# Kernel tuning notes

Hardware: AMD Instinct MI355X
Metric: run time of the kernel (lower is better)

## Reference

```python
import jax, jax.numpy as jnp
import numpy as np
from math import sqrt

B, IN_F, OUT_F = 32, 1024, 4096
DROPOUT_RATE = 0.1


def setup_inputs() -> dict:
    key = jax.random.key(0)
    kx, kw, kb, kmw, kmb = jax.random.split(key, 5)
    k = sqrt(1.0 / IN_F)  # He-style init std from source
    x = jax.random.normal(kx, (B, IN_F), dtype=jnp.float32)
    weight = k * jax.random.normal(kw, (IN_F, OUT_F), dtype=jnp.float32)
    bias = k * jax.random.normal(kb, (OUT_F,), dtype=jnp.float32)
    # per-sample Bernoulli keep masks: rand > dropout_rate (no 1/(1-p) rescale in source)
    w_mask = jax.random.uniform(kmw, (B, IN_F, OUT_F)) > DROPOUT_RATE
    b_mask = jax.random.uniform(kmb, (B, OUT_F)) > DROPOUT_RATE
    return {"x": x, "weight": weight, "bias": bias, "w_mask": w_mask, "b_mask": b_mask}


def reference(x, weight, bias, w_mask, b_mask):
    # 'w' dropout mode: per-sample masked weight matmul, vectorized over batch
    # (replaces the original Python loop of B GEMVs with one batched contraction).
    mw = w_mask.astype(x.dtype)
    y = jnp.einsum("bi,io,bio->bo", x, weight, mw)  # [B, OUT_F]
    return y + bias[None, :] * b_mask.astype(x.dtype)
```

## Files before the change

### kernel.cpp

```cpp
#include <hip/hip_runtime.h>


#define B_DIM 32
#define IN_F 1024
#define OUT_F 4096
#define N_CHUNK 4
#define I_CHUNK (IN_F / N_CHUNK)
#define BO (B_DIM * OUT_F)

typedef int   v4i __attribute__((ext_vector_type(4)));
typedef float v4f __attribute__((ext_vector_type(4)));

__global__ __launch_bounds__(256, 2) void masked_gemv_partial(
    const float* __restrict__ x,
    const float* __restrict__ weight,
    const int* __restrict__ w_mask,
    float* __restrict__ partial)
{
    const int bid   = blockIdx.x;
    const int b     = bid >> 4;
    const int s     = bid & 15;
    const int o_blk = s >> 2;
    const int chunk = s & 3;
    const int i0    = chunk * I_CHUNK;
    const int o     = o_blk * 1024 + (threadIdx.x << 2);

    __shared__ float xs[I_CHUNK];
    xs[threadIdx.x] = x[b * IN_F + i0 + threadIdx.x];
    __syncthreads();

    const int*   mptr = w_mask + (size_t)b * IN_F * OUT_F + (size_t)i0 * OUT_F + o;
    const float* wptr = weight + (size_t)i0 * OUT_F + o;

    v4f acc = {0.f, 0.f, 0.f, 0.f};
#pragma unroll 8
    for (int i = 0; i < I_CHUNK; ++i) {
        const float xi = xs[i];
        const v4i m = __builtin_nontemporal_load((const v4i*)(mptr + (size_t)i * OUT_F));
        const v4f w = *(const v4f*)(wptr + (size_t)i * OUT_F);
        acc.x = fmaf(xi * (float)m.x, w.x, acc.x);
        acc.y = fmaf(xi * (float)m.y, w.y, acc.y);
        acc.z = fmaf(xi * (float)m.z, w.z, acc.z);
        acc.w = fmaf(xi * (float)m.w, w.w, acc.w);
    }

    __builtin_nontemporal_store(acc,
        (v4f*)(partial + (size_t)chunk * BO + b * OUT_F + o));
}

__global__ __launch_bounds__(256) void reduce_bias_kernel(
    const float* __restrict__ partial,
    const float* __restrict__ bias,
    const int* __restrict__ b_mask,
    float* __restrict__ out)
{
    const int tid = blockIdx.x * 256 + threadIdx.x;
    float s0 = partial[tid]               + partial[(size_t)1 * BO + tid];
    float s1 = partial[(size_t)2 * BO + tid] + partial[(size_t)3 * BO + tid];
    const int o = tid & (OUT_F - 1);
    out[tid] = fmaf(bias[o], (float)b_mask[tid], s0 + s1);
}

extern "C" void kernel_launch(void* const* d_in, const int* in_sizes, int n_in,
                              void* d_out, int out_size, void* d_ws, size_t ws_size,
                              hipStream_t stream) {
    const float* x      = (const float*)d_in[0];
    const float* weight = (const float*)d_in[1];
    const float* bias   = (const float*)d_in[2];
    const int*   w_mask = (const int*)d_in[3];
    const int*   b_mask = (const int*)d_in[4];
    float* out     = (float*)d_out;
    float* partial = (float*)d_ws;

    masked_gemv_partial<<<B_DIM * 16, 256, 0, stream>>>(x, weight, w_mask, partial);
    reduce_bias_kernel<<<BO / 256, 256, 0, stream>>>(partial, bias, b_mask, out);
}
```

Baseline: 679.0 us.

## Share weight loads across batch groups and split input dimension into more chunks

Each block now covers 8 batch samples instead of one, so every weight row segment it loads is reused for 8 masked accumulations rather than being read separately per sample. The input dimension is split into 32 chunks instead of 4, giving 512 blocks of short loops. The reduce kernel is vectorized to sum 32 partials with float4 loads. The workload is dominated by the 512MB mask stream, so weight reuse saves little bandwidth, while the partial buffer grows eightfold and each thread now holds 32 accumulator registers.

```diff
diff --git a/kernel.cpp b/kernel.cpp
--- a/kernel.cpp
+++ b/kernel.cpp
@@ -4,7 +4,9 @@
 #define B_DIM 32
 #define IN_F 1024
 #define OUT_F 4096
-#define N_CHUNK 4
+#define BGRP 8
+#define NBG (B_DIM / BGRP)
+#define N_CHUNK 32
 #define I_CHUNK (IN_F / N_CHUNK)
 #define BO (B_DIM * OUT_F)
 
@@ -18,34 +20,48 @@
     float* __restrict__ partial)
 {
     const int bid   = blockIdx.x;
-    const int b     = bid >> 4;
-    const int s     = bid & 15;
-    const int o_blk = s >> 2;
-    const int chunk = s & 3;
+    const int bgrp  = bid >> 7;
+    const int o_blk = (bid >> 5) & 3;
+    const int chunk = bid & 31;
+    const int b0    = bgrp * BGRP;
     const int i0    = chunk * I_CHUNK;
     const int o     = o_blk * 1024 + (threadIdx.x << 2);
 
-    __shared__ float xs[I_CHUNK];
-    xs[threadIdx.x] = x[b * IN_F + i0 + threadIdx.x];
+    __shared__ float xs[BGRP][I_CHUNK];
+    {
+        const int bb = threadIdx.x >> 5;
+        const int ii = threadIdx.x & 31;
+        xs[bb][ii] = x[(b0 + bb) * IN_F + i0 + ii];
+    }
     __syncthreads();
 
-    const int*   mptr = w_mask + (size_t)b * IN_F * OUT_F + (size_t)i0 * OUT_F + o;
     const float* wptr = weight + (size_t)i0 * OUT_F + o;
+    const int*   mbase = w_mask + ((size_t)b0 * IN_F + i0) * OUT_F + o;
 
-    v4f acc = {0.f, 0.f, 0.f, 0.f};
-#pragma unroll 8
+    v4f acc[BGRP];
+#pragma unroll
+    for (int bb = 0; bb < BGRP; ++bb) acc[bb] = (v4f){0.f, 0.f, 0.f, 0.f};
+
+#pragma unroll 2
     for (int i = 0; i < I_CHUNK; ++i) {
-        const float xi = xs[i];
-        const v4i m = __builtin_nontemporal_load((const v4i*)(mptr + (size_t)i * OUT_F));
         const v4f w = *(const v4f*)(wptr + (size_t)i * OUT_F);
-        acc.x = fmaf(xi * (float)m.x, w.x, acc.x);
-        acc.y = fmaf(xi * (float)m.y, w.y, acc.y);
-        acc.z = fmaf(xi * (float)m.z, w.z, acc.z);
-        acc.w = fmaf(xi * (float)m.w, w.w, acc.w);
+#pragma unroll
+        for (int bb = 0; bb < BGRP; ++bb) {
+            const v4i m = __builtin_nontemporal_load(
+                (const v4i*)(mbase + ((size_t)bb * IN_F + i) * OUT_F));
+            const float xi = xs[bb][i];
+            acc[bb].x = fmaf(xi * (float)m.x, w.x, acc[bb].x);
+            acc[bb].y = fmaf(xi * (float)m.y, w.y, acc[bb].y);
+            acc[bb].z = fmaf(xi * (float)m.z, w.z, acc[bb].z);
+            acc[bb].w = fmaf(xi * (float)m.w, w.w, acc[bb].w);
+        }
     }
 
-    __builtin_nontemporal_store(acc,
-        (v4f*)(partial + (size_t)chunk * BO + b * OUT_F + o));
+#pragma unroll
+    for (int bb = 0; bb < BGRP; ++bb) {
+        __builtin_nontemporal_store(acc[bb],
+            (v4f*)(partial + (size_t)chunk * BO + (b0 + bb) * OUT_F + o));
+    }
 }
 
 __global__ __launch_bounds__(256) void reduce_bias_kernel(
@@ -55,10 +71,21 @@
     float* __restrict__ out)
 {
     const int tid = blockIdx.x * 256 + threadIdx.x;
-    float s0 = partial[tid]               + partial[(size_t)1 * BO + tid];
-    float s1 = partial[(size_t)2 * BO + tid] + partial[(size_t)3 * BO + tid];
-    const int o = tid & (OUT_F - 1);
-    out[tid] = fmaf(bias[o], (float)b_mask[tid], s0 + s1);
+    const v4f* p4 = (const v4f*)partial;
+    v4f s = {0.f, 0.f, 0.f, 0.f};
+#pragma unroll
+    for (int c = 0; c < N_CHUNK; ++c) {
+        const v4f v = p4[(size_t)c * (BO / 4) + tid];
+        s.x += v.x; s.y += v.y; s.z += v.z; s.w += v.w;
+    }
+    const v4i bm = ((const v4i*)b_mask)[tid];
+    const v4f bi = ((const v4f*)bias)[tid & (OUT_F / 4 - 1)];
+    v4f r;
+    r.x = fmaf(bi.x, (float)bm.x, s.x);
+    r.y = fmaf(bi.y, (float)bm.y, s.y);
+    r.z = fmaf(bi.z, (float)bm.z, s.z);
+    r.w = fmaf(bi.w, (float)bm.w, s.w);
+    ((v4f*)out)[tid] = r;
 }
 
 extern "C" void kernel_launch(void* const* d_in, const int* in_sizes, int n_in,
@@ -72,6 +99,6 @@
     float* out     = (float*)d_out;
     float* partial = (float*)d_ws;
 
-    masked_gemv_partial<<<B_DIM * 16, 256, 0, stream>>>(x, weight, w_mask, partial);
-    reduce_bias_kernel<<<BO / 256, 256, 0, stream>>>(partial, bias, b_mask, out);
+    masked_gemv_partial<<<NBG * 4 * N_CHUNK, 256, 0, stream>>>(x, weight, w_mask, partial);
+    reduce_bias_kernel<<<BO / 4 / 256, 256, 0, stream>>>(partial, bias, b_mask, out);
 }
```

Measured after the change: 685.3 us. Within noise of the previous version (+0.9%).
